# Kernel optimization log

Hardware: AMD Instinct MI355X
Metric: run time of the kernel (lower is better)

The kernel has to match this reference:

```python
import jax, jax.numpy as jnp
import numpy as np

TOP_K = 5
TEMPERATURE = 0.1
EPS = 1e-12


def _normalize(x):
    # F.normalize(x, dim=-1): x / max(||x||, eps)
    n = jnp.linalg.norm(x, axis=-1, keepdims=True)
    return x / jnp.maximum(n, EPS)


def setup_inputs() -> dict:
    key = jax.random.key(0)
    k1, k2, k3 = jax.random.split(key, 3)
    B, N, D = 1024, 200000, 128
    query = jax.random.normal(k1, (B, D), dtype=jnp.float32)
    # memory bank stores L2-normalized keys (MemoryBank.build applies F.normalize)
    memory = _normalize(jax.random.normal(k2, (N, D), dtype=jnp.float32))
    index_map = jnp.arange(N, dtype=jnp.int64)
    exclude_indices = jax.random.randint(k3, (B,), 0, N, dtype=jnp.int64)
    return {"query": query, "memory": memory, "index_map": index_map,
            "exclude_indices": exclude_indices}


def reference(query, memory, index_map, exclude_indices):
    # cosine similarity: normalize query, memory is already normalized
    qn = _normalize(query)                       # [B, D]
    sim = qn @ memory.T                          # [B, N]
    # exclude own training sample (training-time self-exclusion)
    mask = exclude_indices[:, None] == index_map[None, :]   # [B, N]
    sim = jnp.where(mask, -jnp.inf, sim)
    # top-k (effective_top_k = min(top_k, N-1) = TOP_K here)
    top_sim, top_idx = jax.lax.top_k(sim, TOP_K)             # [B, K]
    weights = jax.nn.softmax(top_sim / TEMPERATURE, axis=-1)  # [B, K]
    vecs = memory[top_idx]                                   # [B, K, D]
    retrieved = jnp.einsum('bk,bkd->bd', weights, vecs)      # weighted sum
    retrieved = _normalize(retrieved)
    distances = 1.0 - top_sim[:, 0]                          # [B]
    return retrieved, distances, weights
```

## Files before the change

kernel.cpp:

```cpp
#include <hip/hip_runtime.h>
#include <hip/hip_bf16.h>
#include <math.h>

#define D128 128
#define TOPK 5
#define NP 200704
#define NCH2 12544
#define NSTRIP 392
#define MARGIN 0.008f
#define CAP 1024
#define SCAP 96
#define SCST 34

typedef __attribute__((ext_vector_type(8))) short short8;
typedef __attribute__((ext_vector_type(4))) float f32x4;

__device__ __forceinline__ short f2bf(float f) {
    union { float f; unsigned u; } c; c.f = f;
    unsigned u = c.u + 0x7FFFu + ((c.u >> 16) & 1u);
    return (short)(u >> 16);
}

__device__ __forceinline__ unsigned pkbf(float x, float y) {
    __hip_bfloat162 h = __float22bfloat162_rn(make_float2(x, y));
    unsigned u; __builtin_memcpy(&u, &h, 4);
    return u;
}
__device__ __forceinline__ unsigned pkh(float a, float b) {
    union { _Float16 h[2]; unsigned u; } c;
    c.h[0] = (_Float16)a; c.h[1] = (_Float16)b; return c.u;
}

template <int NN>
__device__ __forceinline__ void insertg(float (&v)[NN], int (&x)[NN], float nv, int nj) {
    bool g[NN];
    #pragma unroll
    for (int i = 0; i < NN; ++i) g[i] = nv > v[i];
    #pragma unroll
    for (int i = NN - 1; i > 0; --i) {
        v[i] = g[i - 1] ? v[i - 1] : (g[i] ? nv : v[i]);
        x[i] = g[i - 1] ? x[i - 1] : (g[i] ? nj : x[i]);
    }
    v[0] = g[0] ? nv : v[0];
    x[0] = g[0] ? nj : x[0];
}
template <int NN>
__device__ __forceinline__ void insertv(float (&v)[NN], float nv) {
    bool g[NN];
    #pragma unroll
    for (int i = 0; i < NN; ++i) g[i] = nv > v[i];
    #pragma unroll
    for (int i = NN - 1; i > 0; --i)
        v[i] = g[i - 1] ? v[i - 1] : (g[i] ? nv : v[i]);
    v[0] = g[0] ? nv : v[0];
}

__global__ void qnorm_kernel(const float* __restrict__ q, float* __restrict__ qn,
                             short* __restrict__ qbf) {
    int b = blockIdx.x, t = threadIdx.x;
    float v0 = q[(size_t)b * D128 + t];
    float v1 = q[(size_t)b * D128 + t + 64];
    float ss = v0 * v0 + v1 * v1;
    #pragma unroll
    for (int off = 32; off > 0; off >>= 1) ss += __shfl_xor(ss, off, 64);
    float scale = 1.0f / fmaxf(sqrtf(ss), 1e-12f);
    float a0 = v0 * scale, a1 = v1 * scale;
    qn[(size_t)b * D128 + t] = a0;
    qn[(size_t)b * D128 + t + 64] = a1;
    qbf[(size_t)b * D128 + t] = f2bf(a0);
    qbf[(size_t)b * D128 + t + 64] = f2bf(a1);
}

#define MFMA16(a, b, c) __builtin_amdgcn_mfma_f32_16x16x32_bf16(a, b, c, 0, 0, 0)

__global__ __launch_bounds__(256, 3) void simtopk_max(
    const short* __restrict__ qbf, const float* __restrict__ mem,
    _Float16* __restrict__ candT, _Float16* __restrict__ stripT, int N) {
    __shared__ short sK[2][64 * 136];
    __shared__ _Float16 sC[256 * SCST];
    const int b = blockIdx.x;
    const int strip = (b & 7) + ((b >> 5) << 3);
    const int qsg = (b >> 3) & 3;
    const int t = threadIdx.x, w = t >> 6, lane = t & 63;
    const int n = lane & 15, quad = lane >> 4;
    const bool qb0 = (quad & 1) != 0, qb1 = (quad & 2) != 0;
    const int qbase = qsg * 256 + w * 64;

    short8 bq[4][4];
    #pragma unroll
    for (int f = 0; f < 4; ++f) {
        const short* qrow = qbf + (size_t)(qbase + f * 16 + n) * D128 + quad * 8;
        #pragma unroll
        for (int s = 0; s < 4; ++s) bq[f][s] = *(const short8*)(qrow + s * 32);
    }

    const size_t k0 = (size_t)strip * 512;
    const int srow = t >> 4, scol = t & 15;
    const float* gbase = mem + (k0 + srow) * (size_t)D128 + scol * 8;
    const bool tail = (k0 + 512 > (size_t)N);

    float4 fa[8];

    auto loadg = [&](int g) {
        const float* base = gbase + (size_t)g * 64 * D128;
        #pragma unroll
        for (int i = 0; i < 4; ++i) {
            const float4* p = (const float4*)(base + (size_t)i * 16 * D128);
            if (tail) {
                size_t key = k0 + (size_t)(g * 64 + srow + i * 16);
                if (key >= (size_t)N) p = (const float4*)mem;
            }
            fa[2 * i]     = p[0];
            fa[2 * i + 1] = p[1];
        }
    };
    auto storesk = [&](int g, int buf) {
        #pragma unroll
        for (int i = 0; i < 4; ++i) {
            uint4 wv;
            wv.x = pkbf(fa[2 * i].x,     fa[2 * i].y);
            wv.y = pkbf(fa[2 * i].z,     fa[2 * i].w);
            wv.z = pkbf(fa[2 * i + 1].x, fa[2 * i + 1].y);
            wv.w = pkbf(fa[2 * i + 1].z, fa[2 * i + 1].w);
            if (tail && (k0 + (size_t)(g * 64 + srow + i * 16) >= (size_t)N))
                wv = make_uint4(0, 0, 0, 0);
            *((uint4*)&sK[buf][(srow + 16 * i) * 136 + scol * 8]) = wv;
        }
    };

    loadg(0);
    storesk(0, 0);
    __syncthreads();
    loadg(1);

    const int qloc = w * 64 + quad * 16 + n;
    unsigned* sCrow = (unsigned*)((char*)sC + qloc * (SCST * 2));

    for (int round = 0; round < 8; ++round) {
        if (round < 7) storesk(round + 1, (round + 1) & 1);
        if (round < 6) loadg(round + 2);

        const short* kb = sK[round & 1];
        float fin[4];
        #pragma unroll
        for (int tt = 0; tt < 4; ++tt) {
            const short* ab = &kb[(tt * 16 + n) * 136 + quad * 8];
            short8 a0 = *(const short8*)(ab);
            short8 a1 = *(const short8*)(ab + 32);
            short8 a2 = *(const short8*)(ab + 64);
            short8 a3 = *(const short8*)(ab + 96);
            f32x4 c0 = {0.f, 0.f, 0.f, 0.f}, c1 = c0, c2 = c0, c3 = c0;
            c0 = MFMA16(a0, bq[0][0], c0);
            c1 = MFMA16(a0, bq[1][0], c1);
            c2 = MFMA16(a0, bq[2][0], c2);
            c3 = MFMA16(a0, bq[3][0], c3);
            c0 = MFMA16(a1, bq[0][1], c0);
            c1 = MFMA16(a1, bq[1][1], c1);
            c2 = MFMA16(a1, bq[2][1], c2);
            c3 = MFMA16(a1, bq[3][1], c3);
            c0 = MFMA16(a2, bq[0][2], c0);
            c1 = MFMA16(a2, bq[1][2], c1);
            c2 = MFMA16(a2, bq[2][2], c2);
            c3 = MFMA16(a2, bq[3][2], c3);
            c0 = MFMA16(a3, bq[0][3], c0);
            c1 = MFMA16(a3, bq[1][3], c1);
            c2 = MFMA16(a3, bq[2][3], c2);
            c3 = MFMA16(a3, bq[3][3], c3);
            float m0 = fmaxf(fmaxf(c0[0], c0[1]), fmaxf(c0[2], c0[3]));
            float m1 = fmaxf(fmaxf(c1[0], c1[1]), fmaxf(c1[2], c1[3]));
            float m2 = fmaxf(fmaxf(c2[0], c2[1]), fmaxf(c2[2], c2[3]));
            float m3 = fmaxf(fmaxf(c3[0], c3[1]), fmaxf(c3[2], c3[3]));
            float u0 = qb0 ? m1 : m0, u1 = qb0 ? m0 : m1;
            float u2 = qb0 ? m3 : m2, u3 = qb0 ? m2 : m3;
            float v0 = qb1 ? u2 : u0, v1 = qb1 ? u3 : u1;
            float v2 = qb1 ? u0 : u2, v3 = qb1 ? u1 : u3;
            float A = fmaxf(v0, __shfl_xor(v2, 32, 64));
            float B = fmaxf(v1, __shfl_xor(v3, 32, 64));
            fin[tt] = fmaxf(A, __shfl_xor(B, 16, 64));
        }
        sCrow[round * 2]     = pkh(fin[0], fin[1]);
        sCrow[round * 2 + 1] = pkh(fin[2], fin[3]);
        __syncthreads();
    }

    {
        int q = qsg * 256 + t;
        unsigned* gdst = (unsigned*)((short*)candT + (size_t)q * NCH2 + strip * 32);
        const unsigned* row = (const unsigned*)((const char*)sC + t * (SCST * 2));
        float mx = -3e38f;
        #pragma unroll
        for (int j = 0; j < 4; ++j) {
            unsigned u0 = row[4 * j], u1 = row[4 * j + 1];
            unsigned u2 = row[4 * j + 2], u3 = row[4 * j + 3];
            uint4 v; v.x = u0; v.y = u1; v.z = u2; v.w = u3;
            *(uint4*)(gdst + 4 * j) = v;
            unsigned uu[4] = {u0, u1, u2, u3};
            #pragma unroll
            for (int e = 0; e < 4; ++e) {
                unsigned short ha = (unsigned short)(uu[e] & 0xffff);
                unsigned short hb = (unsigned short)(uu[e] >> 16);
                _Float16 f0, f1;
                __builtin_memcpy(&f0, &ha, 2); __builtin_memcpy(&f1, &hb, 2);
                mx = fmaxf(mx, fmaxf((float)f0, (float)f1));
            }
        }
        stripT[(size_t)q * NSTRIP + strip] = (_Float16)mx;
    }
}

__global__ __launch_bounds__(256, 4) void finalize_batch(
    const _Float16* __restrict__ candT, const _Float16* __restrict__ stripT,
    const float* __restrict__ mem, const float* __restrict__ qn,
    const int* __restrict__ index_map, const int* __restrict__ excl,
    float* __restrict__ outR, float* __restrict__ outD, float* __restrict__ outW, int N) {
    const int q = blockIdx.x, t = threadIdx.x;
    const int w = t >> 6, lane = t & 63;

    __shared__ __align__(16) float sQ[D128];
    __shared__ __align__(16) _Float16 sS[NSTRIP];
    __shared__ unsigned short sStr[SCAP];
    __shared__ unsigned short sList[CAP];
    __shared__ int sScnt, sSov, sCnt, sOv;
    __shared__ float sThr;
    __shared__ float sMrg[4 * 6];
    __shared__ float sWv[4 * TOPK];
    __shared__ int   sWk[4 * TOPK];
    __shared__ float sW[TOPK];
    __shared__ int   sJ[TOPK];

    if (t < 128) sQ[t] = qn[(size_t)q * D128 + t];
    if (t == 0) { sScnt = 0; sSov = 0; sCnt = 0; sOv = 0; }
    if (t < NSTRIP / 8)
        *(short8*)(&sS[t * 8]) =
            *(const short8*)((const short*)stripT + (size_t)q * NSTRIP + t * 8);
    __syncthreads();

    float pv[6];
    #pragma unroll
    for (int i = 0; i < 6; ++i) pv[i] = -3e38f;
    for (int i = t; i < NSTRIP; i += 256) {
        float v = (float)sS[i];
        if (v > pv[5]) insertv<6>(pv, v);
    }
    #pragma unroll
    for (int r = 0; r < 6; ++r) {
        float bv = pv[0];
        #pragma unroll
        for (int off = 32; off > 0; off >>= 1) bv = fmaxf(bv, __shfl_xor(bv, off, 64));
        int ml = (pv[0] == bv) ? lane : 64;
        #pragma unroll
        for (int off = 32; off > 0; off >>= 1) ml = min(ml, __shfl_xor(ml, off, 64));
        if (lane == ml) {
            #pragma unroll
            for (int i = 0; i < 5; ++i) pv[i] = pv[i + 1];
            pv[5] = -3e38f;
        }
        if (lane == 0) sMrg[w * 6 + r] = bv;
    }
    __syncthreads();
    if (t == 0) {
        float b6[6];
        #pragma unroll
        for (int i = 0; i < 6; ++i) b6[i] = -3e38f;
        for (int j = 0; j < 24; ++j) {
            float v = sMrg[j];
            if (v > b6[5]) insertv<6>(b6, v);
        }
        sThr = b6[5] - 2.0f * MARGIN;
    }
    __syncthreads();

    const float thr = sThr;
    for (int i = t; i < NSTRIP; i += 256) {
        if ((float)sS[i] >= thr) {
            int p = atomicAdd(&sScnt, 1);
            if (p < SCAP) sStr[p] = (unsigned short)i; else sSov = 1;
        }
    }
    __syncthreads();
    const int scnt = min(sScnt, SCAP);

    if (!sSov) {
        for (int base = 0; base < scnt; base += 8) {
            int si = base + (t >> 5);
            if (si < scnt) {
                int ch = (int)sStr[si] * 32 + (t & 31);
                float v = (float)candT[(size_t)q * NCH2 + ch];
                if (v >= thr) {
                    int p = atomicAdd(&sCnt, 1);
                    if (p < CAP) sList[p] = (unsigned short)ch; else sOv = 1;
                }
            }
        }
    }
    __syncthreads();
    const int ov = (sSov || sOv) ? 1 : 0;
    const int cnt = ov ? NCH2 : min(sCnt, CAP);

    const int exq = excl[q];
    float tv[TOPK]; int ti[TOPK];
    #pragma unroll
    for (int i = 0; i < TOPK; ++i) { tv[i] = -3e38f; ti[i] = -1; }
    const int rounds = (cnt + 15) >> 4;
    for (int r = 0; r < rounds; ++r) {
        int slot = r * 16 + (t >> 4);
        int ch = (slot < cnt) ? (ov ? slot : (int)sList[slot]) : -1;
        int key = ch * 16 + (t & 15);
        float v = -3e38f;
        if (ch >= 0 && key < N && index_map[key] != exq) {
            const float4* mr = (const float4*)(mem + (size_t)key * D128);
            const float4* qv = (const float4*)sQ;
            float acc = 0.f;
            #pragma unroll
            for (int d = 0; d < 32; ++d) {
                float4 a = mr[d], b = qv[d];
                acc += a.x * b.x + a.y * b.y + a.z * b.z + a.w * b.w;
            }
            v = acc;
        }
        if (v > tv[TOPK - 1]) insertg<TOPK>(tv, ti, v, key);
    }

    #pragma unroll
    for (int r = 0; r < TOPK; ++r) {
        float bv = tv[0]; int bk = ti[0];
        #pragma unroll
        for (int off = 32; off > 0; off >>= 1) {
            float ovv = __shfl_xor(bv, off, 64);
            int   okk = __shfl_xor(bk, off, 64);
            if (ovv > bv || (ovv == bv && (unsigned)okk < (unsigned)bk)) { bv = ovv; bk = okk; }
        }
        if (tv[0] == bv && ti[0] == bk) {
            #pragma unroll
            for (int i = 0; i < TOPK - 1; ++i) { tv[i] = tv[i + 1]; ti[i] = ti[i + 1]; }
            tv[TOPK - 1] = -3e38f; ti[TOPK - 1] = -1;
        }
        if (lane == 0) { sWv[w * TOPK + r] = bv; sWk[w * TOPK + r] = bk; }
    }
    __syncthreads();
    if (t == 0) {
        float bv[TOPK]; int bi[TOPK];
        #pragma unroll
        for (int i = 0; i < TOPK; ++i) { bv[i] = -3e38f; bi[i] = -1; }
        for (int j = 0; j < 4 * TOPK; ++j) {
            float v = sWv[j];
            if (v > bv[TOPK - 1]) insertg<TOPK>(bv, bi, v, sWk[j]);
        }
        float m = bv[0], ex[TOPK], sum = 0.f;
        #pragma unroll
        for (int k = 0; k < TOPK; ++k) { ex[k] = __expf((bv[k] - m) * 10.0f); sum += ex[k]; }
        float inv = 1.0f / sum;
        #pragma unroll
        for (int k = 0; k < TOPK; ++k) {
            float wk = ex[k] * inv;
            sW[k] = wk; sJ[k] = bi[k];
            outW[(size_t)q * TOPK + k] = wk;
        }
        outD[q] = 1.0f - bv[0];
    }
    __syncthreads();
    if (t < 64) {
        float r0 = 0.f, r1 = 0.f;
        #pragma unroll
        for (int k = 0; k < TOPK; ++k) {
            const float* mr = mem + (size_t)sJ[k] * D128;
            r0 += sW[k] * mr[t];
            r1 += sW[k] * mr[t + 64];
        }
        float ss = r0 * r0 + r1 * r1;
        #pragma unroll
        for (int off = 32; off > 0; off >>= 1) ss += __shfl_xor(ss, off, 64);
        float scale = 1.0f / fmaxf(sqrtf(ss), 1e-12f);
        outR[(size_t)q * D128 + t]      = r0 * scale;
        outR[(size_t)q * D128 + t + 64] = r1 * scale;
    }
}

extern "C" void kernel_launch(void* const* d_in, const int* in_sizes, int n_in,
                              void* d_out, int out_size, void* d_ws, size_t ws_size,
                              hipStream_t stream) {
    const float* query  = (const float*)d_in[0];
    const float* memory = (const float*)d_in[1];
    const int* index_map = (const int*)d_in[2];
    const int* excl      = (const int*)d_in[3];

    const int B = in_sizes[3];
    const int N = in_sizes[2];

    char* ws = (char*)d_ws;
    float*    qn     = (float*)(ws);
    short*    qbf    = (short*)(ws + 524288);
    _Float16* candT  = (_Float16*)(ws + 786432);
    _Float16* stripT = (_Float16*)(ws + 786432 + 25690112);

    float* outR = (float*)d_out;
    float* outD = outR + (size_t)B * D128;
    float* outW = outD + B;

    qnorm_kernel<<<B, 64, 0, stream>>>(query, qn, qbf);
    simtopk_max<<<NSTRIP * 4, 256, 0, stream>>>(qbf, memory, candT, stripT, N);
    finalize_batch<<<B, 256, 0, stream>>>(candT, stripT, memory, qn, index_map, excl,
                                          outR, outD, outW, N);
}
```

Measured before the change: 247.1 us.

## Use 512-thread blocks covering half the queries, single-buffer key tile

The similarity/max kernel now launches 512-thread blocks that each handle 512 queries against a 512-key strip, halving the number of blocks. Each memory tile is therefore loaded and converted to bf16 once per 512 queries instead of once per 256, which halves global reads of the memory bank. The LDS key buffer goes from double to single buffering and each round adds an extra barrier around the store. The block-to-strip mapping is also reordered. In exchange, global loads overlap less with MFMA work and there are more barriers per round.

```diff
diff --git a/kernel.cpp b/kernel.cpp
--- a/kernel.cpp
+++ b/kernel.cpp
@@ -73,18 +73,19 @@
 
 #define MFMA16(a, b, c) __builtin_amdgcn_mfma_f32_16x16x32_bf16(a, b, c, 0, 0, 0)
 
-__global__ __launch_bounds__(256, 3) void simtopk_max(
+__global__ __launch_bounds__(512, 3) void simtopk_max(
     const short* __restrict__ qbf, const float* __restrict__ mem,
     _Float16* __restrict__ candT, _Float16* __restrict__ stripT, int N) {
-    __shared__ short sK[2][64 * 136];
-    __shared__ _Float16 sC[256 * SCST];
+    __shared__ short sK[64 * 136];
+    __shared__ _Float16 sC[512 * SCST];
     const int b = blockIdx.x;
-    const int strip = (b & 7) + ((b >> 5) << 3);
-    const int qsg = (b >> 3) & 3;
+    const int m = (b & 7) * 98 + (b >> 3);
+    const int strip = m >> 1;
+    const int qh = m & 1;
     const int t = threadIdx.x, w = t >> 6, lane = t & 63;
     const int n = lane & 15, quad = lane >> 4;
     const bool qb0 = (quad & 1) != 0, qb1 = (quad & 2) != 0;
-    const int qbase = qsg * 256 + w * 64;
+    const int qbase = qh * 512 + w * 64;
 
     short8 bq[4][4];
     #pragma unroll
@@ -95,41 +96,33 @@
     }
 
     const size_t k0 = (size_t)strip * 512;
-    const int srow = t >> 4, scol = t & 15;
-    const float* gbase = mem + (k0 + srow) * (size_t)D128 + scol * 8;
+    const int srow = t >> 3, scol = t & 7;
+    const float* gbase = mem + (k0 + srow) * (size_t)D128 + scol * 16;
     const bool tail = (k0 + 512 > (size_t)N);
 
-    float4 fa[8];
+    float4 fa[4];
 
     auto loadg = [&](int g) {
-        const float* base = gbase + (size_t)g * 64 * D128;
-        #pragma unroll
-        for (int i = 0; i < 4; ++i) {
-            const float4* p = (const float4*)(base + (size_t)i * 16 * D128);
-            if (tail) {
-                size_t key = k0 + (size_t)(g * 64 + srow + i * 16);
-                if (key >= (size_t)N) p = (const float4*)mem;
-            }
-            fa[2 * i]     = p[0];
-            fa[2 * i + 1] = p[1];
-        }
+        const float4* p = (const float4*)(gbase + (size_t)g * 64 * D128);
+        if (tail && (k0 + (size_t)(g * 64 + srow) >= (size_t)N))
+            p = (const float4*)mem;
+        fa[0] = p[0]; fa[1] = p[1]; fa[2] = p[2]; fa[3] = p[3];
     };
-    auto storesk = [&](int g, int buf) {
-        #pragma unroll
-        for (int i = 0; i < 4; ++i) {
-            uint4 wv;
-            wv.x = pkbf(fa[2 * i].x,     fa[2 * i].y);
-            wv.y = pkbf(fa[2 * i].z,     fa[2 * i].w);
-            wv.z = pkbf(fa[2 * i + 1].x, fa[2 * i + 1].y);
-            wv.w = pkbf(fa[2 * i + 1].z, fa[2 * i + 1].w);
-            if (tail && (k0 + (size_t)(g * 64 + srow + i * 16) >= (size_t)N))
-                wv = make_uint4(0, 0, 0, 0);
-            *((uint4*)&sK[buf][(srow + 16 * i) * 136 + scol * 8]) = wv;
-        }
+    auto storesk = [&](int g) {
+        uint4 w0, w1;
+        w0.x = pkbf(fa[0].x, fa[0].y); w0.y = pkbf(fa[0].z, fa[0].w);
+        w0.z = pkbf(fa[1].x, fa[1].y); w0.w = pkbf(fa[1].z, fa[1].w);
+        w1.x = pkbf(fa[2].x, fa[2].y); w1.y = pkbf(fa[2].z, fa[2].w);
+        w1.z = pkbf(fa[3].x, fa[3].y); w1.w = pkbf(fa[3].z, fa[3].w);
+        if (tail && (k0 + (size_t)(g * 64 + srow) >= (size_t)N)) {
+            w0 = make_uint4(0, 0, 0, 0); w1 = make_uint4(0, 0, 0, 0);
+        }
+        *((uint4*)&sK[srow * 136 + scol * 16])     = w0;
+        *((uint4*)&sK[srow * 136 + scol * 16 + 8]) = w1;
     };
 
     loadg(0);
-    storesk(0, 0);
+    storesk(0);
     __syncthreads();
     loadg(1);
 
@@ -137,14 +130,10 @@
     unsigned* sCrow = (unsigned*)((char*)sC + qloc * (SCST * 2));
 
     for (int round = 0; round < 8; ++round) {
-        if (round < 7) storesk(round + 1, (round + 1) & 1);
-        if (round < 6) loadg(round + 2);
-
-        const short* kb = sK[round & 1];
         float fin[4];
         #pragma unroll
         for (int tt = 0; tt < 4; ++tt) {
-            const short* ab = &kb[(tt * 16 + n) * 136 + quad * 8];
+            const short* ab = &sK[(tt * 16 + n) * 136 + quad * 8];
             short8 a0 = *(const short8*)(ab);
             short8 a1 = *(const short8*)(ab + 32);
             short8 a2 = *(const short8*)(ab + 64);
@@ -180,11 +169,17 @@
         }
         sCrow[round * 2]     = pkh(fin[0], fin[1]);
         sCrow[round * 2 + 1] = pkh(fin[2], fin[3]);
-        __syncthreads();
-    }
-
+        if (round < 7) {
+            __syncthreads();
+            storesk(round + 1);
+            __syncthreads();
+            if (round < 6) loadg(round + 2);
+        }
+    }
+
+    __syncthreads();
     {
-        int q = qsg * 256 + t;
+        int q = qh * 512 + t;
         unsigned* gdst = (unsigned*)((short*)candT + (size_t)q * NCH2 + strip * 32);
         const unsigned* row = (const unsigned*)((const char*)sC + t * (SCST * 2));
         float mx = -3e38f;
@@ -398,7 +393,7 @@
     float* outW = outD + B;
 
     qnorm_kernel<<<B, 64, 0, stream>>>(query, qn, qbf);
-    simtopk_max<<<NSTRIP * 4, 256, 0, stream>>>(qbf, memory, candT, stripT, N);
+    simtopk_max<<<NSTRIP * 2, 512, 0, stream>>>(qbf, memory, candT, stripT, N);
     finalize_batch<<<B, 256, 0, stream>>>(candT, stripT, memory, qn, index_map, excl,
                                           outR, outD, outW, N);
 }
```

Measured after the change: 252.7 us. 1.02x slower.
